# Performance work log

Measured on AMD Instinct MI355X. Metric: run time of the kernel, lower is better.

Reference implementation:

```python
import jax, jax.numpy as jnp
import numpy as np

B, S, D_IN, D_OUT = 4, 4096, 2048, 2048


def setup_inputs() -> dict:
    key = jax.random.key(0)
    kx, kw = jax.random.split(key)
    x = jax.random.normal(kx, (B, S, D_IN), dtype=jnp.float32)
    weight = jax.random.normal(kw, (D_OUT, D_IN), dtype=jnp.float32) * 0.02
    return {"x": x, "weight": weight}


def reference(x, weight):
    # Per-row absmax int8 activation quantization
    x_scale = jnp.clip(jnp.max(jnp.abs(x), axis=-1, keepdims=True), 1e-05, None)  # [B,S,1]
    x_quant = jnp.clip(jnp.round(x / x_scale * 127.0), -128.0, 127.0)
    # Ternary weight quantization (mean-centered absmean scale)
    w_mean = jnp.mean(weight)
    w_centered = weight - w_mean
    w_scale = jnp.clip(jnp.mean(jnp.abs(w_centered)), 1e-05, None)
    w_quant = jnp.clip(jnp.round(w_centered / w_scale), -1.0, 1.0)
    # GEMM on quantized values, then dequant rescale
    y = jnp.einsum('bsi,oi->bso', x_quant, w_quant)  # [B,S,D_OUT]
    y = y * (w_scale * x_scale / 127.0)
    return y.astype(x.dtype)
```

## Files before the change

kernel.cpp:

```cpp
#include <hip/hip_runtime.h>
#include <stdint.h>

#define M_TOT 16384
#define K_DIM 2048
#define N_DIM 2048
#define W_ELEMS (N_DIM * K_DIM)

typedef int v4i  __attribute__((ext_vector_type(4)));

__device__ __forceinline__ void async_load16(const void* gptr, void* lptr) {
    __builtin_amdgcn_global_load_lds(
        (__attribute__((address_space(1))) void*)(uintptr_t)gptr,
        (__attribute__((address_space(3))) void*)(uint32_t)(uintptr_t)lptr,
        16, 0, 0);
}

__device__ __forceinline__ int qclamp(float v, int lo, int hi) {
    int q = (int)rintf(v);
    q = q > hi ? hi : (q < lo ? lo : q);
    return q & 255;
}

__global__ __launch_bounds__(256) void wsum_kernel(const float* __restrict__ w,
                                                   double* __restrict__ spart) {
    int tid = blockIdx.x * 256 + threadIdx.x;
    const float4* w4 = (const float4*)w;
    double s = 0.0;
    #pragma unroll
    for (int it = 0; it < 8; it++) {
        float4 v = w4[tid + it * 131072];
        s += (double)v.x + (double)v.y + (double)v.z + (double)v.w;
    }
    #pragma unroll
    for (int off = 32; off; off >>= 1) s += __shfl_down(s, off);
    __shared__ double ls[4];
    if ((threadIdx.x & 63) == 0) ls[threadIdx.x >> 6] = s;
    __syncthreads();
    if (threadIdx.x == 0) spart[blockIdx.x] = ls[0] + ls[1] + ls[2] + ls[3];
}

__global__ __launch_bounds__(256) void wabs_kernel(const float* __restrict__ w,
                                                   const double* __restrict__ spart,
                                                   double* __restrict__ apart) {
    __shared__ double ls[4];
    double sm = spart[threadIdx.x] + spart[threadIdx.x + 256];
    #pragma unroll
    for (int off = 32; off; off >>= 1) sm += __shfl_down(sm, off);
    if ((threadIdx.x & 63) == 0) ls[threadIdx.x >> 6] = sm;
    __syncthreads();
    double mean = (ls[0] + ls[1] + ls[2] + ls[3]) * (1.0 / (double)W_ELEMS);
    __syncthreads();
    int tid = blockIdx.x * 256 + threadIdx.x;
    const float4* w4 = (const float4*)w;
    double s = 0.0;
    #pragma unroll
    for (int it = 0; it < 8; it++) {
        float4 v = w4[tid + it * 131072];
        s += fabs((double)v.x - mean) + fabs((double)v.y - mean) +
             fabs((double)v.z - mean) + fabs((double)v.w - mean);
    }
    #pragma unroll
    for (int off = 32; off; off >>= 1) s += __shfl_down(s, off);
    if ((threadIdx.x & 63) == 0) ls[threadIdx.x >> 6] = s;
    __syncthreads();
    if (threadIdx.x == 0) apart[blockIdx.x] = ls[0] + ls[1] + ls[2] + ls[3];
}

__global__ __launch_bounds__(256) void quant_kernel(
    const float* __restrict__ x, const float* __restrict__ w,
    const double* __restrict__ spart, const double* __restrict__ apart,
    int8_t* __restrict__ xq, int8_t* __restrict__ wq,
    float* __restrict__ xscale, float* __restrict__ wsf)
{
    const int t = threadIdx.x;
    if (blockIdx.x < 4096) {
        const int row  = (blockIdx.x << 2) | (t >> 6);
        const int lane = t & 63;
        const float4* xr = (const float4*)(x + (size_t)row * K_DIM);
        float4 v[8];
        #pragma unroll
        for (int i = 0; i < 8; i++) v[i] = xr[lane + (i << 6)];
        float m = 0.0f;
        #pragma unroll
        for (int i = 0; i < 8; i++)
            m = fmaxf(m, fmaxf(fmaxf(fabsf(v[i].x), fabsf(v[i].y)),
                               fmaxf(fabsf(v[i].z), fabsf(v[i].w))));
        #pragma unroll
        for (int off = 32; off; off >>= 1) m = fmaxf(m, __shfl_xor(m, off));
        const float scale = fmaxf(m, 1e-5f);
        if (lane == 0) xscale[row] = scale;
        int* outp = (int*)(xq + (size_t)row * K_DIM);
        #pragma unroll
        for (int i = 0; i < 8; i++) {
            int p = qclamp(v[i].x / scale * 127.0f, -128, 127)
                  | (qclamp(v[i].y / scale * 127.0f, -128, 127) << 8)
                  | (qclamp(v[i].z / scale * 127.0f, -128, 127) << 16)
                  | (qclamp(v[i].w / scale * 127.0f, -128, 127) << 24);
            outp[lane + (i << 6)] = p;
        }
    } else {
        __shared__ double ls0[4], ls1[4];
        double s0 = spart[t] + spart[t + 256];
        double s1 = apart[t] + apart[t + 256];
        #pragma unroll
        for (int off = 32; off; off >>= 1) {
            s0 += __shfl_down(s0, off);
            s1 += __shfl_down(s1, off);
        }
        if ((t & 63) == 0) { ls0[t >> 6] = s0; ls1[t >> 6] = s1; }
        __syncthreads();
        float mean  = (float)((ls0[0] + ls0[1] + ls0[2] + ls0[3]) * (1.0 / (double)W_ELEMS));
        float scale = (float)fmax((ls1[0] + ls1[1] + ls1[2] + ls1[3]) * (1.0 / (double)W_ELEMS), 1e-5);
        int i = (blockIdx.x - 4096) * 256 + t;
        float4 v = ((const float4*)w)[i];
        int p = qclamp((v.x - mean) / scale, -1, 1)
              | (qclamp((v.y - mean) / scale, -1, 1) << 8)
              | (qclamp((v.z - mean) / scale, -1, 1) << 16)
              | (qclamp((v.w - mean) / scale, -1, 1) << 24);
        ((int*)wq)[i] = p;
        if (i == 0) wsf[0] = scale * (1.0f / 127.0f);
    }
}

__global__ __launch_bounds__(512, 2) void gemm_i8_kernel(
    const int8_t* __restrict__ xq, const int8_t* __restrict__ wq,
    const float* __restrict__ xscale, const float* __restrict__ wsf,
    float* __restrict__ out)
{
    __shared__ __align__(16) int8_t lsA[2][16384];
    __shared__ __align__(16) int8_t lsB[2][16384];

    const int tid  = threadIdx.x;
    const int lane = tid & 63;
    const int wv   = tid >> 6;

    const int flat = blockIdx.x;
    const int nf   = ((flat & 7) << 6) | (flat >> 3);
    const int bm   = nf >> 3;
    const int bn   = nf & 7;

    const int sChunk = (((tid & 3) ^ ((tid >> 3) & 3)) << 4);
    const int8_t* gAb = xq + (size_t)(bm * 256 + (tid >> 2)) * K_DIM + sChunk;
    const int8_t* gBb = wq + (size_t)(bn * 256 + (tid >> 2)) * K_DIM + sChunk;

    #define STAGE(NB, K0)                                                      \
        do {                                                                   \
            async_load16(gAb + (K0),                       lsA[NB] + tid * 16);\
            async_load16(gAb + (K0) + (size_t)128 * K_DIM, lsA[NB] + 8192 + tid * 16); \
            async_load16(gBb + (K0),                       lsB[NB] + tid * 16);\
            async_load16(gBb + (K0) + (size_t)128 * K_DIM, lsB[NB] + 8192 + tid * 16); \
        } while (0)

    const int wm = (wv >> 2) << 7;
    const int wn = (wv & 3) << 6;
    const int fr = lane & 15;
    const int fc = lane >> 4;
    int aoff[8], boff[4];
    #pragma unroll
    for (int mi = 0; mi < 8; mi++) {
        int ra = wm + mi * 16 + fr;
        aoff[mi] = ra * 64 + ((fc ^ ((ra >> 1) & 3)) << 4);
    }
    #pragma unroll
    for (int nj = 0; nj < 4; nj++) {
        int rb = wn + nj * 16 + fr;
        boff[nj] = rb * 64 + ((fc ^ ((rb >> 1) & 3)) << 4);
    }

    v4i acc[8][4] = {};

    #define TILE(CB, T)                                                        \
        do {                                                                   \
            if ((T) < 31) STAGE((CB) ^ 1, ((T) + 1) << 6);                     \
            v4i af[8], bf[4];                                                  \
            _Pragma("unroll")                                                  \
            for (int mi_ = 0; mi_ < 8; mi_++)                                  \
                af[mi_] = *(const v4i*)(lsA[CB] + aoff[mi_]);                  \
            _Pragma("unroll")                                                  \
            for (int nj_ = 0; nj_ < 4; nj_++)                                  \
                bf[nj_] = *(const v4i*)(lsB[CB] + boff[nj_]);                  \
            __builtin_amdgcn_s_setprio(1);                                     \
            _Pragma("unroll")                                                  \
            for (int mi_ = 0; mi_ < 8; mi_++)                                  \
                _Pragma("unroll")                                              \
                for (int nj_ = 0; nj_ < 4; nj_++)                              \
                    acc[mi_][nj_] = __builtin_amdgcn_mfma_i32_16x16x64_i8(     \
                        af[mi_], bf[nj_], acc[mi_][nj_], 0, 0, 0);             \
            __builtin_amdgcn_s_setprio(0);                                     \
            asm volatile("s_waitcnt vmcnt(0) lgkmcnt(0)" ::: "memory");        \
            __builtin_amdgcn_s_barrier();                                      \
        } while (0)

    STAGE(0, 0);
    asm volatile("s_waitcnt vmcnt(0)" ::: "memory");
    __builtin_amdgcn_s_barrier();

    for (int t = 0; t < 32; t += 2) {
        TILE(0, t);
        TILE(1, t + 1);
    }
    #undef TILE
    #undef STAGE

    const float f127 = wsf[0];
    #pragma unroll
    for (int mi = 0; mi < 8; mi++) {
        #pragma unroll
        for (int rg = 0; rg < 4; rg++) {
            const int mg = bm * 256 + wm + mi * 16 + (lane >> 4) * 4 + rg;
            const float fs = f127 * xscale[mg];
            float* orow = out + (size_t)mg * N_DIM + bn * 256 + wn;
            #pragma unroll
            for (int nj = 0; nj < 4; nj++)
                orow[nj * 16 + fr] = fs * (float)acc[mi][nj][rg];
        }
    }
}

extern "C" void kernel_launch(void* const* d_in, const int* in_sizes, int n_in,
                              void* d_out, int out_size, void* d_ws, size_t ws_size,
                              hipStream_t stream) {
    const float* x = (const float*)d_in[0];
    const float* w = (const float*)d_in[1];
    float* out = (float*)d_out;

    char* ws = (char*)d_ws;
    double* spart  = (double*)ws;
    double* apart  = (double*)(ws + 4096);
    float*  wsf    = (float*)(ws + 8192);
    float*  xscale = (float*)(ws + 12288);
    int8_t* xq     = (int8_t*)(ws + 12288 + 65536);
    int8_t* wq     = xq + (size_t)M_TOT * K_DIM;

    wsum_kernel <<<512, 256, 0, stream>>>(w, spart);
    wabs_kernel <<<512, 256, 0, stream>>>(w, spart, apart);
    quant_kernel<<<8192, 256, 0, stream>>>(x, w, spart, apart, xq, wq, xscale, wsf);
    gemm_i8_kernel<<<512, 512, 0, stream>>>(xq, wq, xscale, wsf, out);
}
```

Measured before the change: 308.8 us.

## Triple-buffer GEMM LDS tiles with two-deep prefetch and reciprocal quant scaling

The int8 GEMM goes from double to triple buffering in LDS. It prefetches two K-tiles ahead and waits with vmcnt(4) instead of draining all loads each iteration, so global-to-LDS loads overlap with MFMA work across tiles. The quantization kernels also replace per-element divisions with a multiply by a precomputed reciprocal. In exchange, LDS per block grows from 64KB to 96KB, which likely stops two 512-thread blocks from sharing a CU, and the reciprocal multiply can shift rounding on a few quantized values.

```diff
diff --git a/kernel.cpp b/kernel.cpp
--- a/kernel.cpp
+++ b/kernel.cpp
@@ -89,13 +89,14 @@
         for (int off = 32; off; off >>= 1) m = fmaxf(m, __shfl_xor(m, off));
         const float scale = fmaxf(m, 1e-5f);
         if (lane == 0) xscale[row] = scale;
+        const float rs = 127.0f / scale;
         int* outp = (int*)(xq + (size_t)row * K_DIM);
         #pragma unroll
         for (int i = 0; i < 8; i++) {
-            int p = qclamp(v[i].x / scale * 127.0f, -128, 127)
-                  | (qclamp(v[i].y / scale * 127.0f, -128, 127) << 8)
-                  | (qclamp(v[i].z / scale * 127.0f, -128, 127) << 16)
-                  | (qclamp(v[i].w / scale * 127.0f, -128, 127) << 24);
+            int p = qclamp(v[i].x * rs, -128, 127)
+                  | (qclamp(v[i].y * rs, -128, 127) << 8)
+                  | (qclamp(v[i].z * rs, -128, 127) << 16)
+                  | (qclamp(v[i].w * rs, -128, 127) << 24);
             outp[lane + (i << 6)] = p;
         }
     } else {
@@ -111,12 +112,13 @@
         __syncthreads();
         float mean  = (float)((ls0[0] + ls0[1] + ls0[2] + ls0[3]) * (1.0 / (double)W_ELEMS));
         float scale = (float)fmax((ls1[0] + ls1[1] + ls1[2] + ls1[3]) * (1.0 / (double)W_ELEMS), 1e-5);
+        const float ri = 1.0f / scale;
         int i = (blockIdx.x - 4096) * 256 + t;
         float4 v = ((const float4*)w)[i];
-        int p = qclamp((v.x - mean) / scale, -1, 1)
-              | (qclamp((v.y - mean) / scale, -1, 1) << 8)
-              | (qclamp((v.z - mean) / scale, -1, 1) << 16)
-              | (qclamp((v.w - mean) / scale, -1, 1) << 24);
+        int p = qclamp((v.x - mean) * ri, -1, 1)
+              | (qclamp((v.y - mean) * ri, -1, 1) << 8)
+              | (qclamp((v.z - mean) * ri, -1, 1) << 16)
+              | (qclamp((v.w - mean) * ri, -1, 1) << 24);
         ((int*)wq)[i] = p;
         if (i == 0) wsf[0] = scale * (1.0f / 127.0f);
     }
@@ -127,8 +129,8 @@
     const float* __restrict__ xscale, const float* __restrict__ wsf,
     float* __restrict__ out)
 {
-    __shared__ __align__(16) int8_t lsA[2][16384];
-    __shared__ __align__(16) int8_t lsB[2][16384];
+    __shared__ __align__(16) int8_t lsA[3][16384];
+    __shared__ __align__(16) int8_t lsB[3][16384];
 
     const int tid  = threadIdx.x;
     const int lane = tid & 63;
@@ -143,12 +145,12 @@
     const int8_t* gAb = xq + (size_t)(bm * 256 + (tid >> 2)) * K_DIM + sChunk;
     const int8_t* gBb = wq + (size_t)(bn * 256 + (tid >> 2)) * K_DIM + sChunk;
 
-    #define STAGE(NB, K0)                                                      \
+    #define STAGE(NB, T)                                                       \
         do {                                                                   \
-            async_load16(gAb + (K0),                       lsA[NB] + tid * 16);\
-            async_load16(gAb + (K0) + (size_t)128 * K_DIM, lsA[NB] + 8192 + tid * 16); \
-            async_load16(gBb + (K0),                       lsB[NB] + tid * 16);\
-            async_load16(gBb + (K0) + (size_t)128 * K_DIM, lsB[NB] + 8192 + tid * 16); \
+            async_load16(gAb + ((T) << 6),                       lsA[NB] + tid * 16); \
+            async_load16(gAb + ((T) << 6) + (size_t)128 * K_DIM, lsA[NB] + 8192 + tid * 16); \
+            async_load16(gBb + ((T) << 6),                       lsB[NB] + tid * 16); \
+            async_load16(gBb + ((T) << 6) + (size_t)128 * K_DIM, lsB[NB] + 8192 + tid * 16); \
         } while (0)
 
     const int wm = (wv >> 2) << 7;
@@ -169,9 +171,8 @@
 
     v4i acc[8][4] = {};
 
-    #define TILE(CB, T)                                                        \
+    #define COMPUTE(CB)                                                        \
         do {                                                                   \
-            if ((T) < 31) STAGE((CB) ^ 1, ((T) + 1) << 6);                     \
             v4i af[8], bf[4];                                                  \
             _Pragma("unroll")                                                  \
             for (int mi_ = 0; mi_ < 8; mi_++)                                  \
@@ -187,19 +188,33 @@
                     acc[mi_][nj_] = __builtin_amdgcn_mfma_i32_16x16x64_i8(     \
                         af[mi_], bf[nj_], acc[mi_][nj_], 0, 0, 0);             \
             __builtin_amdgcn_s_setprio(0);                                     \
-            asm volatile("s_waitcnt vmcnt(0) lgkmcnt(0)" ::: "memory");        \
+        } while (0)
+
+    #define TILE_MID(CB, NB, T)                                                \
+        do {                                                                   \
+            STAGE(NB, (T) + 2);                                                \
+            COMPUTE(CB);                                                       \
+            asm volatile("s_waitcnt vmcnt(4)" ::: "memory");                   \
             __builtin_amdgcn_s_barrier();                                      \
         } while (0)
 
     STAGE(0, 0);
+    STAGE(1, 1);
+    asm volatile("s_waitcnt vmcnt(4)" ::: "memory");
+    __builtin_amdgcn_s_barrier();
+
+    for (int tt = 0; tt < 30; tt += 3) {
+        TILE_MID(0, 2, tt);
+        TILE_MID(1, 0, tt + 1);
+        TILE_MID(2, 1, tt + 2);
+    }
+    COMPUTE(0);
     asm volatile("s_waitcnt vmcnt(0)" ::: "memory");
     __builtin_amdgcn_s_barrier();
-
-    for (int t = 0; t < 32; t += 2) {
-        TILE(0, t);
-        TILE(1, t + 1);
-    }
-    #undef TILE
+    COMPUTE(1);
+
+    #undef TILE_MID
+    #undef COMPUTE
     #undef STAGE
 
     const float f127 = wsf[0];
```

After: 307.9 us. About the same (-0.3%).

## Load B fragments directly from a pre-tiled weight layout, triple-buffer A in LDS

Applied to the files above, without the earlier changes.

The weight quantization kernel now writes int8 weights in an MFMA-fragment-friendly tiled layout, so the GEMM can load B operand fragments straight from global memory into registers (double-buffered in registers) instead of staging them through LDS. The A tile moves to a three-stage LDS ring with a partial vmcnt wait, so prefetch runs two tiles ahead. This halves LDS traffic per tile and relaxes the full-drain barrier. The cost is more register pressure, since B comes from global/L2 per wave with possible latency exposure, and every wave loads its own B fragments redundantly.

```diff
diff --git a/kernel.cpp b/kernel.cpp
--- a/kernel.cpp
+++ b/kernel.cpp
@@ -117,7 +117,9 @@
               | (qclamp((v.y - mean) / scale, -1, 1) << 8)
               | (qclamp((v.z - mean) / scale, -1, 1) << 16)
               | (qclamp((v.w - mean) / scale, -1, 1) << 24);
-        ((int*)wq)[i] = p;
+        const int o  = i >> 9;
+        const int kw = i & 511;
+        ((int*)wq)[((o >> 5) << 14) + ((kw >> 2) << 7) + ((o & 31) << 2) + (kw & 3)] = p;
         if (i == 0) wsf[0] = scale * (1.0f / 127.0f);
     }
 }
@@ -127,8 +129,7 @@
     const float* __restrict__ xscale, const float* __restrict__ wsf,
     float* __restrict__ out)
 {
-    __shared__ __align__(16) int8_t lsA[2][16384];
-    __shared__ __align__(16) int8_t lsB[2][16384];
+    __shared__ __align__(16) int8_t lsA[3][16384];
 
     const int tid  = threadIdx.x;
     const int lane = tid & 63;
@@ -141,66 +142,88 @@
 
     const int sChunk = (((tid & 3) ^ ((tid >> 3) & 3)) << 4);
     const int8_t* gAb = xq + (size_t)(bm * 256 + (tid >> 2)) * K_DIM + sChunk;
-    const int8_t* gBb = wq + (size_t)(bn * 256 + (tid >> 2)) * K_DIM + sChunk;
-
-    #define STAGE(NB, K0)                                                      \
-        do {                                                                   \
-            async_load16(gAb + (K0),                       lsA[NB] + tid * 16);\
-            async_load16(gAb + (K0) + (size_t)128 * K_DIM, lsA[NB] + 8192 + tid * 16); \
-            async_load16(gBb + (K0),                       lsB[NB] + tid * 16);\
-            async_load16(gBb + (K0) + (size_t)128 * K_DIM, lsB[NB] + 8192 + tid * 16); \
+
+    #define STAGE_A(NB, T)                                                     \
+        do {                                                                   \
+            async_load16(gAb + ((size_t)(T) << 6),       lsA[NB] + tid * 16);  \
+            async_load16(gAb + ((size_t)(T) << 6) + (size_t)128 * K_DIM,       \
+                         lsA[NB] + 8192 + tid * 16);                           \
         } while (0)
 
     const int wm = (wv >> 2) << 7;
     const int wn = (wv & 3) << 6;
     const int fr = lane & 15;
     const int fc = lane >> 4;
-    int aoff[8], boff[4];
+    int aoff[8];
     #pragma unroll
     for (int mi = 0; mi < 8; mi++) {
         int ra = wm + mi * 16 + fr;
         aoff[mi] = ra * 64 + ((fc ^ ((ra >> 1) & 3)) << 4);
     }
-    #pragma unroll
-    for (int nj = 0; nj < 4; nj++) {
-        int rb = wn + nj * 16 + fr;
-        boff[nj] = rb * 64 + ((fc ^ ((rb >> 1) & 3)) << 4);
-    }
+
+    const int8_t* gB = wq + (((size_t)((bn * 256 + wn) >> 5)) << 16)
+                          + (fc << 9) + (fr << 4);
+    v4i bf0[4], bf1[4];
+    #define LOADB(DST, T)                                                      \
+        do {                                                                   \
+            const int8_t* p_ = gB + ((size_t)(T) << 11);                       \
+            DST[0] = *(const v4i*)(p_);                                        \
+            DST[1] = *(const v4i*)(p_ + 256);                                  \
+            DST[2] = *(const v4i*)(p_ + 65536);                                \
+            DST[3] = *(const v4i*)(p_ + 65536 + 256);                          \
+        } while (0)
 
     v4i acc[8][4] = {};
 
-    #define TILE(CB, T)                                                        \
-        do {                                                                   \
-            if ((T) < 31) STAGE((CB) ^ 1, ((T) + 1) << 6);                     \
-            v4i af[8], bf[4];                                                  \
+    #define COMPUTE(CURB, BC)                                                  \
+        do {                                                                   \
+            v4i af[8];                                                         \
             _Pragma("unroll")                                                  \
             for (int mi_ = 0; mi_ < 8; mi_++)                                  \
-                af[mi_] = *(const v4i*)(lsA[CB] + aoff[mi_]);                  \
-            _Pragma("unroll")                                                  \
-            for (int nj_ = 0; nj_ < 4; nj_++)                                  \
-                bf[nj_] = *(const v4i*)(lsB[CB] + boff[nj_]);                  \
+                af[mi_] = *(const v4i*)(lsA[CURB] + aoff[mi_]);                \
             __builtin_amdgcn_s_setprio(1);                                     \
             _Pragma("unroll")                                                  \
             for (int mi_ = 0; mi_ < 8; mi_++)                                  \
                 _Pragma("unroll")                                              \
                 for (int nj_ = 0; nj_ < 4; nj_++)                              \
                     acc[mi_][nj_] = __builtin_amdgcn_mfma_i32_16x16x64_i8(     \
-                        af[mi_], bf[nj_], acc[mi_][nj_], 0, 0, 0);             \
+                        af[mi_], BC[nj_], acc[mi_][nj_], 0, 0, 0);             \
             __builtin_amdgcn_s_setprio(0);                                     \
-            asm volatile("s_waitcnt vmcnt(0) lgkmcnt(0)" ::: "memory");        \
+        } while (0)
+
+    #define TILE(T, CURB, STB, BC, BN)                                         \
+        do {                                                                   \
+            LOADB(BN, (T) + 1);                                                \
+            STAGE_A(STB, (T) + 2);                                             \
+            COMPUTE(CURB, BC);                                                 \
+            asm volatile("s_waitcnt vmcnt(2)" ::: "memory");                   \
             __builtin_amdgcn_s_barrier();                                      \
         } while (0)
 
-    STAGE(0, 0);
+    STAGE_A(0, 0);
+    LOADB(bf0, 0);
+    STAGE_A(1, 1);
+    asm volatile("s_waitcnt vmcnt(2)" ::: "memory");
+    __builtin_amdgcn_s_barrier();
+
+    for (int tt = 0; tt < 30; tt += 6) {
+        TILE(tt,     0, 2, bf0, bf1);
+        TILE(tt + 1, 1, 0, bf1, bf0);
+        TILE(tt + 2, 2, 1, bf0, bf1);
+        TILE(tt + 3, 0, 2, bf1, bf0);
+        TILE(tt + 4, 1, 0, bf0, bf1);
+        TILE(tt + 5, 2, 1, bf1, bf0);
+    }
+    LOADB(bf1, 31);
+    COMPUTE(0, bf0);
     asm volatile("s_waitcnt vmcnt(0)" ::: "memory");
     __builtin_amdgcn_s_barrier();
-
-    for (int t = 0; t < 32; t += 2) {
-        TILE(0, t);
-        TILE(1, t + 1);
-    }
+    COMPUTE(1, bf1);
+
     #undef TILE
-    #undef STAGE
+    #undef COMPUTE
+    #undef LOADB
+    #undef STAGE_A
 
     const float f127 = wsf[0];
     #pragma unroll
```

After: 312.9 us. No clear change (+1.3%).
